# Optimization experiments

Hardware: AMD Instinct MI355X
Metric: run time of the kernel (lower is better)

The kernel has to match this reference:

```python
import jax, jax.numpy as jnp
import numpy as np

N = 100000      # nodes
EG = 600000     # global (knn) edges used by GAT layers
E = 600000      # prediction edges scored by edge_mlp
H = 1           # gat_heads
C = 64          # hidden_dim (per-head out channels)
HC = H * C
EDGE_IN = 2 * HC + 2  # 130
EDGE_HID = EDGE_IN * 4  # 520


def gat_layer(x, W, att_src, att_dst, bias, src, dst):
    # PyG GATConv (concat=True, residual=False, no edge_dim, eval mode)
    n = x.shape[0]
    h = (x @ W).reshape(n, H, C)                      # [N,H,C]
    a_s = jnp.sum(h * att_src, axis=-1)               # [N,H]
    a_d = jnp.sum(h * att_dst, axis=-1)               # [N,H]
    alpha = jax.nn.leaky_relu(a_s[src] + a_d[dst], 0.2)  # [Eg,H]
    amax = jax.ops.segment_max(alpha, dst, num_segments=n)
    amax = jnp.where(jnp.isfinite(amax), amax, 0.0)
    e = jnp.exp(alpha - amax[dst])
    denom = jax.ops.segment_sum(e, dst, num_segments=n)
    w = e / (denom[dst] + 1e-16)                      # scatter-softmax over in-edges of dst
    out = jax.ops.segment_sum(h[src] * w[:, :, None], dst, num_segments=n)
    return out.reshape(n, HC) + bias


def setup_inputs() -> dict:
    key = jax.random.key(0)
    ks = jax.random.split(key, 16)
    glorot = lambda k, shape: jax.random.normal(k, shape, jnp.float32) * np.sqrt(2.0 / (shape[0] + shape[-1]))
    inp = {
        "pos": jax.random.normal(ks[0], (N, 3), jnp.float32),
        "edge_index": jax.random.randint(ks[1], (2, E), 0, N, jnp.int32),
        "global_edge_index": jax.random.randint(ks[2], (2, EG), 0, N, jnp.int32),
        "edge_attr": jax.random.uniform(ks[3], (E, 2), jnp.float32),
        # GAT layer 0 (in=3)
        "W0": glorot(ks[4], (3, HC)),
        "att_src0": glorot(ks[5], (1, H, C)),
        "att_dst0": glorot(ks[6], (1, H, C)),
        "b0": jnp.zeros((HC,), jnp.float32),
        # GAT layer 1 (in=HC)
        "W1": glorot(ks[7], (HC, HC)),
        "att_src1": glorot(ks[8], (1, H, C)),
        "att_dst1": glorot(ks[9], (1, H, C)),
        "b1": jnp.zeros((HC,), jnp.float32),
        # edge MLP: Linear(130,520) -> ELU -> Linear(520,1)
        "Wm1": glorot(ks[10], (EDGE_IN, EDGE_HID)),
        "bm1": jnp.zeros((EDGE_HID,), jnp.float32),
        "Wm2": glorot(ks[11], (EDGE_HID, 1)),
        "bm2": jnp.zeros((1,), jnp.float32),
    }
    return inp


def reference(pos, edge_index, global_edge_index, edge_attr,
              W0, att_src0, att_dst0, b0,
              W1, att_src1, att_dst1, b1,
              Wm1, bm1, Wm2, bm2):
    gsrc, gdst = global_edge_index[0], global_edge_index[1]
    x = pos  # dropout p=0 -> identity
    x = jax.nn.elu(gat_layer(x, W0, att_src0, att_dst0, b0, gsrc, gdst))
    x = jax.nn.elu(gat_layer(x, W1, att_src1, att_dst1, b1, gsrc, gdst))
    # per-edge gather-concat-MLP
    esrc, edst = edge_index[0], edge_index[1]
    ef = jnp.concatenate([x[esrc], x[edst], edge_attr], axis=1)  # [E, 130]
    h = jax.nn.elu(ef @ Wm1 + bm1)
    edge_values = (h @ Wm2 + bm2)[:, 0]  # [E]
    return edge_values
```

## Files before the change

### kernel.cpp

```cpp
#include <hip/hip_runtime.h>

#define KN 100000
#define KEG 600000
#define KE 600000
#define NB 98
#define LOG2E 1.4426950408889634f
#define LN2 0.6931471805599453f

#define FB_PREP 391
#define FB_CVEC 33
#define FB_HIST 2344
#define FB_T0 25000

using u16 = unsigned short;
typedef __bf16 bf16x8 __attribute__((ext_vector_type(8)));
typedef float f32x4 __attribute__((ext_vector_type(4)));
typedef float f32x2 __attribute__((ext_vector_type(2)));

__device__ __forceinline__ float b2f(u16 u) { return __uint_as_float(((unsigned)u) << 16); }
__device__ __forceinline__ u16 f2b(float f) {
  unsigned u = __float_as_uint(f);
  u += 0x7FFF + ((u >> 16) & 1);
  return (u16)(u >> 16);
}
__device__ __forceinline__ int imin(int a, int b) { return a < b ? a : b; }
__device__ __forceinline__ float fexp2(float x) {
#if __has_builtin(__builtin_amdgcn_exp2f)
  return __builtin_amdgcn_exp2f(x);
#else
  return __expf(x * LN2);
#endif
}

__device__ __forceinline__ void gload_lds16(const void* g, void* l) {
  __builtin_amdgcn_global_load_lds(
      (const __attribute__((address_space(1))) unsigned int*)g,
      (__attribute__((address_space(3))) unsigned int*)l,
      16, 0, 0);
}

__global__ __launch_bounds__(256) void k_front(
    const float* __restrict__ pos, const float* __restrict__ W0,
    const float* __restrict__ att_s, const float* __restrict__ att_d,
    const float* __restrict__ wm1, const float* __restrict__ bm1,
    const float* __restrict__ wm2, const float* __restrict__ w1,
    const int* __restrict__ gdst,
    u16* __restrict__ wm1t, u16* __restrict__ w1t, float2* __restrict__ wsc2,
    float* __restrict__ w2sum, int* __restrict__ counts,
    u16* __restrict__ h, float* __restrict__ a_s, float* __restrict__ a_d) {
  int bid = blockIdx.x;
  if (bid < FB_PREP) {
    int idx = bid * 256 + threadIdx.x;
    if (idx < 33 * 5 * 512) {
      int j = idx & 7;
      int lane = (idx >> 3) & 63;
      int f = (idx >> 9) % 5;
      int nt = idx / (512 * 5);
      int n = nt * 16 + (lane & 15);
      float v = 0.f;
      if (n < 520) {
        if (f < 4) {
          int k = f * 32 + (lane >> 4) * 8 + j;
          v = wm1[k * 520 + n] * LOG2E;
        } else {
          int kk = (lane >> 4) * 8 + j;
          if (kk == 0) v = wm1[128 * 520 + n] * LOG2E;
          else if (kk == 1) v = wm1[129 * 520 + n] * LOG2E;
          else if (kk == 2) v = bm1[n] * LOG2E;
        }
      }
      wm1t[idx] = f2b(v);
    }
    if (idx < 33 * 64) {
      int lane = idx & 63, nt = idx >> 6;
      int col = nt * 16 + (lane & 15);
      float w2 = (col < 520) ? wm2[col] : 0.f;
      float2 p; p.x = w2; p.y = -LN2 * w2;
      wsc2[idx] = p;
    }
    if (idx < 4 * 2 * 64 * 8) {
      int j = idx & 7;
      int lane = (idx >> 3) & 63;
      int kt = (idx >> 9) & 1;
      int nt = idx >> 10;
      int n = nt * 16 + (lane & 15);
      int k = kt * 32 + (lane >> 4) * 8 + j;
      w1t[idx] = f2b(w1[k * 64 + n]);
    }
  } else if (bid < FB_PREP + FB_CVEC) {
    int lane = threadIdx.x & 63;
    int w = (bid - FB_PREP) * 4 + (threadIdx.x >> 6);
    float x = 0.f;
    if (w <= 129) {
      const float* row = wm1 + (size_t)w * 520;
#pragma unroll
      for (int j = 0; j < 8; ++j) x += row[j * 64 + lane] * wm2[j * 64 + lane];
      if (lane < 8) x += row[512 + lane] * wm2[512 + lane];
    } else if (w == 130) {
#pragma unroll
      for (int j = 0; j < 8; ++j) x += bm1[j * 64 + lane] * wm2[j * 64 + lane];
      if (lane < 8) x += bm1[512 + lane] * wm2[512 + lane];
    } else if (w == 131) {
#pragma unroll
      for (int j = 0; j < 8; ++j) x += wm2[j * 64 + lane];
      if (lane < 8) x += wm2[512 + lane];
    }
    for (int off = 1; off < 64; off <<= 1) x += __shfl_xor(x, off);
    if (w <= 130 && lane < 16) {
      int f = w >> 5, kk = w & 31;
      int qq = kk >> 3, jj = kk & 7;
      u16 chi = f2b(x);
      float v = (lane == 0) ? x : (lane == 1 ? (x - b2f(chi)) : 0.f);
      wm1t[(33 * 5 + f) * 512 + (qq * 16 + lane) * 8 + jj] = f2b(v);
    } else if (w == 131 && lane == 0) {
      w2sum[0] = x;
    }
  } else if (bid < FB_PREP + FB_CVEC + FB_HIST) {
    int e = (bid - (FB_PREP + FB_CVEC)) * 256 + threadIdx.x;
    if (e < KEG) atomicAdd(counts + gdst[e], 1);
  } else {
    int lane = threadIdx.x & 63;
    int n = (bid - (FB_PREP + FB_CVEC + FB_HIST)) * 4 + (threadIdx.x >> 6);
    float p0 = pos[n * 3 + 0], p1 = pos[n * 3 + 1], p2 = pos[n * 3 + 2];
    float hv = p0 * W0[lane] + p1 * W0[64 + lane] + p2 * W0[128 + lane];
    h[n * 64 + lane] = f2b(hv);
    float s = hv * att_s[lane];
    float d = hv * att_d[lane];
    for (int off = 1; off < 64; off <<= 1) { s += __shfl_xor(s, off); d += __shfl_xor(d, off); }
    if (lane == 0) { a_s[n] = s; a_d[n] = d; }
  }
}


__global__ __launch_bounds__(1024) void k_scan_block(
    const int* __restrict__ counts, int* __restrict__ incl, int* __restrict__ bsum) {
  int gid = blockIdx.x * 1024 + threadIdx.x;
  int lane = threadIdx.x & 63, w = threadIdx.x >> 6;
  int x = (gid < KN) ? counts[gid] : 0;
  for (int off = 1; off < 64; off <<= 1) {
    int y = __shfl_up(x, off);
    if (lane >= off) x += y;
  }
  __shared__ int wtot[16];
  if (lane == 63) wtot[w] = x;
  __syncthreads();
  if (w == 0 && lane < 16) {
    int t = wtot[lane];
    for (int off = 1; off < 16; off <<= 1) {
      int y = __shfl_up(t, off);
      if (lane >= off) t += y;
    }
    wtot[lane] = t;
  }
  __syncthreads();
  if (w > 0) x += wtot[w - 1];
  if (gid < KN) incl[gid] = x;
  if (threadIdx.x == 1023) bsum[blockIdx.x] = x;
}

__global__ __launch_bounds__(64) void k_scan_bsum(const int* __restrict__ bsum, int* __restrict__ boff) {
  int lane = threadIdx.x;
  int x0 = (lane < NB) ? bsum[lane] : 0;
  int x1 = (64 + lane < NB) ? bsum[64 + lane] : 0;
  int i0 = x0, i1 = x1;
  for (int off = 1; off < 64; off <<= 1) {
    int y0 = __shfl_up(i0, off), y1 = __shfl_up(i1, off);
    if (lane >= off) { i0 += y0; i1 += y1; }
  }
  int tot0 = __shfl(i0, 63);
  if (lane < NB) boff[lane] = i0 - x0;
  if (64 + lane < NB) boff[64 + lane] = i1 - x1 + tot0;
}

__global__ __launch_bounds__(1024) void k_scan_final(
    const int* __restrict__ incl, const int* __restrict__ counts,
    const int* __restrict__ boff, int* __restrict__ row_start) {
  int gid = blockIdx.x * 1024 + threadIdx.x;
  if (gid < KN) row_start[gid] = incl[gid] - counts[gid] + boff[blockIdx.x];
}

__global__ __launch_bounds__(256) void k_fill(
    const int* __restrict__ gsrc, const int* __restrict__ gdst,
    const int* __restrict__ row_start, int* __restrict__ cursor,
    int* __restrict__ csr_src) {
  int e = blockIdx.x * 256 + threadIdx.x;
  if (e >= KEG) return;
  int d = gdst[e];
  int pos = atomicAdd(cursor + d, 1);
  csr_src[row_start[d] + pos] = gsrc[e];
}


__global__ __launch_bounds__(256) void k_aggt1(
    const int* __restrict__ row_start, const int* __restrict__ counts,
    const int* __restrict__ csr_src, const float* __restrict__ a_s0,
    const float* __restrict__ a_d0, const u16* __restrict__ h0,
    const float* __restrict__ b0, const u16* __restrict__ w1t,
    const float* __restrict__ as1, const float* __restrict__ ad1,
    u16* __restrict__ h1, float* __restrict__ a_s1, float* __restrict__ a_d1) {
  __shared__ u16 xb[64][72];
  int lane = threadIdx.x & 63;
  int wave = threadIdx.x >> 6;
  int nb = blockIdx.x * 64;
  int nodebase = nb + wave * 16;

  for (int i = 0; i < 16; ++i) {
    int n = nodebase + i;
    float v = 0.f;
    if (n < KN) {
      int start = row_start[n], deg = counts[n];
      float adn = a_d0[n];
      float acc = 0.f, den = 0.f;
      int j = 0;
      for (; j + 4 <= deg; j += 4) {
        int s0 = csr_src[start + j];
        int s1 = csr_src[start + j + 1];
        int s2 = csr_src[start + j + 2];
        int s3 = csr_src[start + j + 3];
        float al0 = a_s0[s0] + adn; al0 = al0 > 0.f ? al0 : 0.2f * al0;
        float al1 = a_s0[s1] + adn; al1 = al1 > 0.f ? al1 : 0.2f * al1;
        float al2 = a_s0[s2] + adn; al2 = al2 > 0.f ? al2 : 0.2f * al2;
        float al3 = a_s0[s3] + adn; al3 = al3 > 0.f ? al3 : 0.2f * al3;
        float w0 = __expf(al0), w1 = __expf(al1);
        float w2 = __expf(al2), w3 = __expf(al3);
        float h0v = b2f(h0[s0 * 64 + lane]);
        float h1v = b2f(h0[s1 * 64 + lane]);
        float h2v = b2f(h0[s2 * 64 + lane]);
        float h3v = b2f(h0[s3 * 64 + lane]);
        den += (w0 + w1) + (w2 + w3);
        acc += w0 * h0v + w1 * h1v + w2 * h2v + w3 * h3v;
      }
      for (; j < deg; ++j) {
        int s0 = csr_src[start + j];
        float al = a_s0[s0] + adn; al = al > 0.f ? al : 0.2f * al;
        float w0 = __expf(al);
        den += w0;
        acc += w0 * b2f(h0[s0 * 64 + lane]);
      }
      v = acc / (den + 1e-16f) + b0[lane];
      v = v > 0.f ? v : expm1f(v);
    }
    xb[wave * 16 + i][lane] = f2b(v);
  }

  int m = lane & 15, q = lane >> 4;
  const u16* row = xb[wave * 16 + m];
  bf16x8 A0 = *(const bf16x8*)(row + q * 8);
  bf16x8 A1 = *(const bf16x8*)(row + 32 + q * 8);

  const bf16x8* bt = (const bf16x8*)w1t;
  float ps[4] = {0.f, 0.f, 0.f, 0.f};
  float pd[4] = {0.f, 0.f, 0.f, 0.f};
#pragma unroll
  for (int nt = 0; nt < 4; ++nt) {
    int col = nt * 16 + m;
    float asv = as1[col], adv = ad1[col];
    f32x4 acc = {0.f, 0.f, 0.f, 0.f};
    acc = __builtin_amdgcn_mfma_f32_16x16x32_bf16(A0, bt[(nt * 2 + 0) * 64 + lane], acc, 0, 0, 0);
    acc = __builtin_amdgcn_mfma_f32_16x16x32_bf16(A1, bt[(nt * 2 + 1) * 64 + lane], acc, 0, 0, 0);
#pragma unroll
    for (int r = 0; r < 4; ++r) {
      int rown = nodebase + q * 4 + r;
      if (rown < KN) h1[rown * 64 + col] = f2b(acc[r]);
      ps[r] += acc[r] * asv;
      pd[r] += acc[r] * adv;
    }
  }
#pragma unroll
  for (int r = 0; r < 4; ++r) {
    float s = ps[r], d = pd[r];
    s += __shfl_xor(s, 1); d += __shfl_xor(d, 1);
    s += __shfl_xor(s, 2); d += __shfl_xor(d, 2);
    s += __shfl_xor(s, 4); d += __shfl_xor(d, 4);
    s += __shfl_xor(s, 8); d += __shfl_xor(d, 8);
    int rown = nodebase + q * 4 + r;
    if (m == 0 && rown < KN) { a_s1[rown] = s; a_d1[rown] = d; }
  }
}

__global__ __launch_bounds__(256) void k_gat_agg(
    const int* __restrict__ row_start, const int* __restrict__ counts,
    const int* __restrict__ csr_src, const float* __restrict__ a_s,
    const float* __restrict__ a_d, const u16* __restrict__ h,
    const float* __restrict__ bias, u16* __restrict__ xout) {
  int lane = threadIdx.x & 63;
  int n = blockIdx.x * 4 + (threadIdx.x >> 6);
  int start = row_start[n], deg = counts[n];
  float adn = a_d[n];
  float acc = 0.f, den = 0.f;
  int j = 0;
  for (; j + 4 <= deg; j += 4) {
    int s0 = csr_src[start + j];
    int s1 = csr_src[start + j + 1];
    int s2 = csr_src[start + j + 2];
    int s3 = csr_src[start + j + 3];
    float al0 = a_s[s0] + adn; al0 = al0 > 0.f ? al0 : 0.2f * al0;
    float al1 = a_s[s1] + adn; al1 = al1 > 0.f ? al1 : 0.2f * al1;
    float al2 = a_s[s2] + adn; al2 = al2 > 0.f ? al2 : 0.2f * al2;
    float al3 = a_s[s3] + adn; al3 = al3 > 0.f ? al3 : 0.2f * al3;
    float w0 = __expf(al0), w1 = __expf(al1);
    float w2 = __expf(al2), w3 = __expf(al3);
    float h0 = b2f(h[s0 * 64 + lane]);
    float h1 = b2f(h[s1 * 64 + lane]);
    float h2 = b2f(h[s2 * 64 + lane]);
    float h3 = b2f(h[s3 * 64 + lane]);
    den += (w0 + w1) + (w2 + w3);
    acc += w0 * h0 + w1 * h1 + w2 * h2 + w3 * h3;
  }
  for (; j < deg; ++j) {
    int s0 = csr_src[start + j];
    float al = a_s[s0] + adn; al = al > 0.f ? al : 0.2f * al;
    float w0 = __expf(al);
    den += w0;
    acc += w0 * b2f(h[s0 * 64 + lane]);
  }
  float v = acc / (den + 1e-16f) + bias[lane];
  v = v > 0.f ? v : expm1f(v);
  xout[n * 64 + lane] = f2b(v);
}

__global__ __launch_bounds__(256) void k_edge_mlp(
    const int* __restrict__ eidx, const u16* __restrict__ x2bf,
    const float* __restrict__ eattr, const u16* __restrict__ wm1t,
    const float2* __restrict__ wsc2, const float* __restrict__ w2sum,
    const float* __restrict__ bm2, float* __restrict__ out) {
  __shared__ uint4 Bbuf[2][1408];
  int tid = threadIdx.x;
  int lane = tid & 63;
  int wave = tid >> 6;
  int base = blockIdx.x * 256 + wave * 64;
  int m = lane & 15, q = lane >> 4;

  bf16x8 A[4][4];
#pragma unroll
  for (int s = 0; s < 4; ++s) {
    int row = imin(base + s * 16 + m, KE - 1);
    int es = eidx[row], ed = eidx[KE + row];
    const bf16x8* psrc = (const bf16x8*)(x2bf + es * 64);
    const bf16x8* pdst = (const bf16x8*)(x2bf + ed * 64);
    A[s][0] = psrc[q];
    A[s][1] = psrc[q + 4];
    A[s][2] = pdst[q];
    A[s][3] = pdst[q + 4];
  }
  bf16x8 A5[4];
#pragma unroll
  for (int s = 0; s < 4; ++s) {
    bf16x8 a5 = {0, 0, 0, 0, 0, 0, 0, 0};
    if (q == 0) {
      int row = imin(base + s * 16 + m, KE - 1);
      a5[0] = (__bf16)eattr[row * 2 + 0];
      a5[1] = (__bf16)eattr[row * 2 + 1];
      a5[2] = (__bf16)1.0f;
    }
    A5[s] = a5;
  }

  const uint4* gB = (const uint4*)wm1t;
  const uint4* gW = (const uint4*)wsc2;
#pragma unroll
  for (int k = 0; k < 5; ++k)
    gload_lds16(gB + tid + k * 256, &Bbuf[0][tid + k * 256]);
  gload_lds16(gW + lane, &Bbuf[0][1280 + lane]);
  gload_lds16(gW + 64 + lane, &Bbuf[0][1280 + 64 + lane]);

  f32x2 osum[4][2];
#pragma unroll
  for (int s = 0; s < 4; ++s) {
    osum[s][0] = (f32x2){0.f, 0.f};
    osum[s][1] = (f32x2){0.f, 0.f};
  }

#pragma unroll 1
  for (int ch = 0; ch < 9; ++ch) {
    int cur = ch & 1, nxt = cur ^ 1;
    if (ch > 0) __builtin_amdgcn_s_barrier();
    if (ch < 8) {
      const uint4* gs = gB + (ch + 1) * 1280;
#pragma unroll
      for (int k = 0; k < 5; ++k)
        gload_lds16(gs + tid + k * 256, &Bbuf[nxt][tid + k * 256]);
      const uint4* ws = gW + (ch + 1) * 128;
      gload_lds16(ws + lane, &Bbuf[nxt][1280 + lane]);
      gload_lds16(ws + 64 + lane, &Bbuf[nxt][1280 + 64 + lane]);
      asm volatile("s_waitcnt vmcnt(7)" ::: "memory");
    } else {
      asm volatile("s_waitcnt vmcnt(0)" ::: "memory");
    }
    __builtin_amdgcn_s_barrier();

    int lim = (ch == 8) ? 1 : 4;
#pragma unroll 1
    for (int li = 0; li < lim; ++li) {
      int nt = ch * 4 + li;
      (void)nt;
      const bf16x8* lb = (const bf16x8*)(Bbuf[cur] + li * 5 * 64);
      bf16x8 B0 = lb[0 * 64 + lane];
      bf16x8 B1 = lb[1 * 64 + lane];
      bf16x8 B2 = lb[2 * 64 + lane];
      bf16x8 B3 = lb[3 * 64 + lane];
      bf16x8 B4 = lb[4 * 64 + lane];
      float2 w2 = ((const float2*)(Bbuf[cur] + 1280))[li * 64 + lane];
#pragma unroll
      for (int s = 0; s < 4; ++s) {
        f32x4 acc = {0.f, 0.f, 0.f, 0.f};
        acc = __builtin_amdgcn_mfma_f32_16x16x32_bf16(A[s][0], B0, acc, 0, 0, 0);
        acc = __builtin_amdgcn_mfma_f32_16x16x32_bf16(A[s][1], B1, acc, 0, 0, 0);
        acc = __builtin_amdgcn_mfma_f32_16x16x32_bf16(A[s][2], B2, acc, 0, 0, 0);
        acc = __builtin_amdgcn_mfma_f32_16x16x32_bf16(A[s][3], B3, acc, 0, 0, 0);
        acc = __builtin_amdgcn_mfma_f32_16x16x32_bf16(A5[s],   B4, acc, 0, 0, 0);
        f32x2 t0 = {fminf(acc[0], 0.f), fminf(acc[1], 0.f)};
        f32x2 t1 = {fminf(acc[2], 0.f), fminf(acc[3], 0.f)};
        f32x2 e0 = {fexp2(t0.x), fexp2(t0.y)};
        f32x2 e1 = {fexp2(t1.x), fexp2(t1.y)};
        osum[s][0] += e0 * w2.x + t0 * w2.y;
        osum[s][1] += e1 * w2.x + t1 * w2.y;
      }
    }
  }

  const bf16x8* bt = (const bf16x8*)wm1t;
  bf16x8 L0 = bt[(33 * 5 + 0) * 64 + lane];
  bf16x8 L1 = bt[(33 * 5 + 1) * 64 + lane];
  bf16x8 L2 = bt[(33 * 5 + 2) * 64 + lane];
  bf16x8 L3 = bt[(33 * 5 + 3) * 64 + lane];
  bf16x8 L4 = bt[(33 * 5 + 4) * 64 + lane];
  float w2s = w2sum[0];
  float b2v = bm2[0];

#pragma unroll
  for (int s = 0; s < 4; ++s) {
    f32x4 accL = {0.f, 0.f, 0.f, 0.f};
    accL = __builtin_amdgcn_mfma_f32_16x16x32_bf16(A[s][0], L0, accL, 0, 0, 0);
    accL = __builtin_amdgcn_mfma_f32_16x16x32_bf16(A[s][1], L1, accL, 0, 0, 0);
    accL = __builtin_amdgcn_mfma_f32_16x16x32_bf16(A[s][2], L2, accL, 0, 0, 0);
    accL = __builtin_amdgcn_mfma_f32_16x16x32_bf16(A[s][3], L3, accL, 0, 0, 0);
    accL = __builtin_amdgcn_mfma_f32_16x16x32_bf16(A5[s],   L4, accL, 0, 0, 0);
    float ov[4] = {osum[s][0].x, osum[s][0].y, osum[s][1].x, osum[s][1].y};
#pragma unroll
    for (int r = 0; r < 4; ++r) {
      float lin = accL[r] + __shfl_xor(accL[r], 1);
      float v = ov[r];
      v += __shfl_xor(v, 1);
      v += __shfl_xor(v, 2);
      v += __shfl_xor(v, 4);
      v += __shfl_xor(v, 8);
      if (m == 0) {
        int row = base + s * 16 + q * 4 + r;
        if (row < KE) out[row] = v - w2s + lin + b2v;
      }
    }
  }
}

extern "C" void kernel_launch(void* const* d_in, const int* in_sizes, int n_in,
                              void* d_out, int out_size, void* d_ws, size_t ws_size,
                              hipStream_t stream) {
  const float* pos  = (const float*)d_in[0];
  const int* eidx   = (const int*)d_in[1];
  const int* geidx  = (const int*)d_in[2];
  const float* eattr= (const float*)d_in[3];
  const float* W0   = (const float*)d_in[4];
  const float* as0  = (const float*)d_in[5];
  const float* ad0  = (const float*)d_in[6];
  const float* b0   = (const float*)d_in[7];
  const float* W1   = (const float*)d_in[8];
  const float* as1  = (const float*)d_in[9];
  const float* ad1  = (const float*)d_in[10];
  const float* b1   = (const float*)d_in[11];
  const float* Wm1  = (const float*)d_in[12];
  const float* bm1  = (const float*)d_in[13];
  const float* Wm2  = (const float*)d_in[14];
  const float* bm2  = (const float*)d_in[15];
  float* out = (float*)d_out;

  char* ws = (char*)d_ws;
  size_t off = 0;
  auto carve = [&](size_t bytes) {
    char* p = ws + off;
    off = (off + bytes + 255) & ~(size_t)255;
    return p;
  };
  int* counts    = (int*)carve((size_t)KN * 4);
  int* cursor    = (int*)carve((size_t)KN * 4);
  int* incl      = (int*)carve((size_t)KN * 4);
  int* row_start = (int*)carve((size_t)KN * 4);
  int* bsum      = (int*)carve(128 * 4);
  int* boff      = (int*)carve(128 * 4);
  int* csr_src   = (int*)carve((size_t)KEG * 4);
  u16* h0        = (u16*)carve((size_t)KN * 64 * 2);
  u16* h1        = (u16*)carve((size_t)KN * 64 * 2);
  u16* x12       = (u16*)carve((size_t)KN * 64 * 2);
  float* a_s0    = (float*)carve((size_t)KN * 4);
  float* a_d0    = (float*)carve((size_t)KN * 4);
  float* a_s1    = (float*)carve((size_t)KN * 4);
  float* a_d1    = (float*)carve((size_t)KN * 4);
  u16* wm1t      = (u16*)carve((size_t)36 * 5 * 512 * 2);
  u16* w1t       = (u16*)carve((size_t)4 * 2 * 64 * 8 * 2);
  float2* wsc2   = (float2*)carve((size_t)36 * 64 * 8);
  float* w2sum   = (float*)carve(256);

  const int* gsrc = geidx;
  const int* gdst = geidx + KEG;

  hipMemsetAsync(d_ws, 0, 800128, stream);

  k_front<<<FB_PREP + FB_CVEC + FB_HIST + FB_T0, 256, 0, stream>>>(
      pos, W0, as0, ad0, Wm1, bm1, Wm2, W1, gdst,
      wm1t, w1t, wsc2, w2sum, counts, h0, a_s0, a_d0);

  k_scan_block<<<NB, 1024, 0, stream>>>(counts, incl, bsum);
  k_scan_bsum<<<1, 64, 0, stream>>>(bsum, boff);
  k_scan_final<<<NB, 1024, 0, stream>>>(incl, counts, boff, row_start);
  k_fill<<<(KEG + 255) / 256, 256, 0, stream>>>(gsrc, gdst, row_start, cursor, csr_src);

  k_aggt1<<<(KN + 63) / 64, 256, 0, stream>>>(row_start, counts, csr_src,
                                              a_s0, a_d0, h0, b0,
                                              w1t, as1, ad1, h1, a_s1, a_d1);

  k_gat_agg<<<KN / 4, 256, 0, stream>>>(row_start, counts, csr_src, a_s1, a_d1, h1, b1, x12);

  k_edge_mlp<<<(KE + 255) / 256, 256, 0, stream>>>(eidx, x12, eattr, wm1t, wsc2, w2sum, bm2, out);
}
```

Measured before the change: 379.9 us.

## Fuse CSR scan and fill stages into one cooperative kernel with grid syncs

Replaces the four-kernel CSR build (block scan, block-sum scan, final offsets, edge fill) with a single cooperative kernel of 98 blocks that uses grid-wide syncs between phases. The per-node inclusive scan stays in registers, so the incl buffer and its reload go away. The goal is to remove three kernel launches and their gaps. The trade-off is that grid.sync barriers are added and the fill phase runs on only 98 blocks looping over edges, which may cut the parallelism available for the atomic scatter.

```diff
diff --git a/kernel.cpp b/kernel.cpp
--- a/kernel.cpp
+++ b/kernel.cpp
@@ -1,4 +1,7 @@
 #include <hip/hip_runtime.h>
+#include <hip/hip_cooperative_groups.h>
+
+namespace cg = cooperative_groups;
 
 #define KN 100000
 #define KEG 600000
@@ -131,12 +134,17 @@
   }
 }
 
-
-__global__ __launch_bounds__(1024) void k_scan_block(
-    const int* __restrict__ counts, int* __restrict__ incl, int* __restrict__ bsum) {
+__global__ __launch_bounds__(1024) void k_csr(
+    const int* __restrict__ counts, int* __restrict__ bsum,
+    int* __restrict__ boff, int* __restrict__ row_start,
+    const int* __restrict__ gsrc, const int* __restrict__ gdst,
+    int* __restrict__ cursor, int* __restrict__ csr_src) {
+  cg::grid_group grid = cg::this_grid();
   int gid = blockIdx.x * 1024 + threadIdx.x;
   int lane = threadIdx.x & 63, w = threadIdx.x >> 6;
-  int x = (gid < KN) ? counts[gid] : 0;
+
+  int c = (gid < KN) ? counts[gid] : 0;
+  int x = c;
   for (int off = 1; off < 64; off <<= 1) {
     int y = __shfl_up(x, off);
     if (lane >= off) x += y;
@@ -154,40 +162,42 @@
   }
   __syncthreads();
   if (w > 0) x += wtot[w - 1];
-  if (gid < KN) incl[gid] = x;
   if (threadIdx.x == 1023) bsum[blockIdx.x] = x;
-}
-
-__global__ __launch_bounds__(64) void k_scan_bsum(const int* __restrict__ bsum, int* __restrict__ boff) {
-  int lane = threadIdx.x;
-  int x0 = (lane < NB) ? bsum[lane] : 0;
-  int x1 = (64 + lane < NB) ? bsum[64 + lane] : 0;
-  int i0 = x0, i1 = x1;
-  for (int off = 1; off < 64; off <<= 1) {
-    int y0 = __shfl_up(i0, off), y1 = __shfl_up(i1, off);
-    if (lane >= off) { i0 += y0; i1 += y1; }
-  }
-  int tot0 = __shfl(i0, 63);
-  if (lane < NB) boff[lane] = i0 - x0;
-  if (64 + lane < NB) boff[64 + lane] = i1 - x1 + tot0;
-}
-
-__global__ __launch_bounds__(1024) void k_scan_final(
-    const int* __restrict__ incl, const int* __restrict__ counts,
-    const int* __restrict__ boff, int* __restrict__ row_start) {
-  int gid = blockIdx.x * 1024 + threadIdx.x;
-  if (gid < KN) row_start[gid] = incl[gid] - counts[gid] + boff[blockIdx.x];
-}
-
-__global__ __launch_bounds__(256) void k_fill(
-    const int* __restrict__ gsrc, const int* __restrict__ gdst,
-    const int* __restrict__ row_start, int* __restrict__ cursor,
-    int* __restrict__ csr_src) {
-  int e = blockIdx.x * 256 + threadIdx.x;
-  if (e >= KEG) return;
-  int d = gdst[e];
-  int pos = atomicAdd(cursor + d, 1);
-  csr_src[row_start[d] + pos] = gsrc[e];
+
+  __threadfence();
+  grid.sync();
+
+  if (blockIdx.x == 0 && threadIdx.x < 64) {
+    int l2 = threadIdx.x;
+    int x0 = (l2 < NB) ? bsum[l2] : 0;
+    int x1 = (64 + l2 < NB) ? bsum[64 + l2] : 0;
+    int i0 = x0, i1 = x1;
+    for (int off = 1; off < 64; off <<= 1) {
+      int y0 = __shfl_up(i0, off), y1 = __shfl_up(i1, off);
+      if (l2 >= off) { i0 += y0; i1 += y1; }
+    }
+    int tot0 = __shfl(i0, 63);
+    if (l2 < NB) boff[l2] = i0 - x0;
+    if (64 + l2 < NB) boff[64 + l2] = i1 - x1 + tot0;
+  }
+
+  __threadfence();
+  grid.sync();
+
+  if (gid < KN) row_start[gid] = x - c + boff[blockIdx.x];
+
+  __threadfence();
+  grid.sync();
+
+#pragma unroll
+  for (int it = 0; it < 6; ++it) {
+    int e = gid + it * (NB * 1024);
+    if (e < KEG) {
+      int d = gdst[e];
+      int pos = atomicAdd(cursor + d, 1);
+      csr_src[row_start[d] + pos] = gsrc[e];
+    }
+  }
 }
 
 
@@ -392,8 +402,6 @@
     int lim = (ch == 8) ? 1 : 4;
 #pragma unroll 1
     for (int li = 0; li < lim; ++li) {
-      int nt = ch * 4 + li;
-      (void)nt;
       const bf16x8* lb = (const bf16x8*)(Bbuf[cur] + li * 5 * 64);
       bf16x8 B0 = lb[0 * 64 + lane];
       bf16x8 B1 = lb[1 * 64 + lane];
@@ -483,7 +491,6 @@
   };
   int* counts    = (int*)carve((size_t)KN * 4);
   int* cursor    = (int*)carve((size_t)KN * 4);
-  int* incl      = (int*)carve((size_t)KN * 4);
   int* row_start = (int*)carve((size_t)KN * 4);
   int* bsum      = (int*)carve(128 * 4);
   int* boff      = (int*)carve(128 * 4);
@@ -509,10 +516,12 @@
       pos, W0, as0, ad0, Wm1, bm1, Wm2, W1, gdst,
       wm1t, w1t, wsc2, w2sum, counts, h0, a_s0, a_d0);
 
-  k_scan_block<<<NB, 1024, 0, stream>>>(counts, incl, bsum);
-  k_scan_bsum<<<1, 64, 0, stream>>>(bsum, boff);
-  k_scan_final<<<NB, 1024, 0, stream>>>(incl, counts, boff, row_start);
-  k_fill<<<(KEG + 255) / 256, 256, 0, stream>>>(gsrc, gdst, row_start, cursor, csr_src);
+  {
+    void* args[] = {(void*)&counts, (void*)&bsum, (void*)&boff,
+                    (void*)&row_start, (void*)&gsrc, (void*)&gdst,
+                    (void*)&cursor, (void*)&csr_src};
+    hipLaunchCooperativeKernel((void*)k_csr, dim3(NB), dim3(1024), args, 0, stream);
+  }
 
   k_aggt1<<<(KN + 63) / 64, 256, 0, stream>>>(row_start, counts, csr_src,
                                               a_s0, a_d0, h0, b0,
```

Result: slower. 525.3 us (+38.3%).
